# Kernel optimization log

Hardware: AMD Instinct MI355X
Metric: run time of the kernel (lower is better)

## Reference

```python
import jax, jax.numpy as jnp
import numpy as np

N_NODES = 50000
N_EDGES = 800000
D_IN = 256
D_OUT = 128
EPS = 1e-9


def setup_inputs() -> dict:
    key = jax.random.key(0)
    ks = jax.random.split(key, 6)
    feat = jax.random.normal(ks[0], (N_NODES, D_IN), dtype=jnp.float32)
    edge_row = jax.random.randint(ks[1], (N_EDGES,), 0, N_NODES)
    edge_col = jax.random.randint(ks[2], (N_EDGES,), 0, N_NODES)
    # normalized adjacency values (positive, ~1/degree scale)
    edge_val = jax.random.uniform(ks[3], (N_EDGES,), dtype=jnp.float32) / 16.0
    # xavier_uniform for Linear(dim_in, dim_out) weights, stored as [D_IN, D_OUT]
    limit = float(np.sqrt(6.0 / (D_IN + D_OUT)))
    W0 = jax.random.uniform(ks[4], (D_IN, D_OUT), minval=-limit, maxval=limit, dtype=jnp.float32)
    W1 = jax.random.uniform(ks[5], (D_IN, D_OUT), minval=-limit, maxval=limit, dtype=jnp.float32)
    zeros = jnp.zeros((D_OUT,), dtype=jnp.float32)
    ones = jnp.ones((D_OUT,), dtype=jnp.float32)
    return {
        "feat": feat,
        "W0": W0, "b0": zeros, "scale0": ones, "offset0": zeros,
        "W1": W1, "b1": zeros, "scale1": ones, "offset1": zeros,
        "edge_row": edge_row, "edge_col": edge_col, "edge_val": edge_val,
    }


def _spmm(edge_row, edge_col, edge_val, x):
    # out[r] += val * x[c] for each edge (r, c, val)  -- sparse adj @ x
    msgs = edge_val[:, None] * x[edge_col]  # [E, D]
    return jax.ops.segment_sum(msgs, edge_row, num_segments=N_NODES)


def _feat_trans(x, W, b, scale, offset):
    h = jax.nn.relu(x @ W + b)  # [N, D_OUT]
    mean = jnp.mean(h, axis=1, keepdims=True)
    var = jnp.var(h, axis=1, keepdims=True) + EPS  # unbiased=False (population var)
    return (h - mean) * scale * jax.lax.rsqrt(var) + offset


def reference(feat, W0, b0, scale0, offset0, W1, b1, scale1, offset1,
              edge_row, edge_col, edge_val):
    # non-first-layer path: feat_hop = [X, A @ X] (order=1), dropout p=0 is identity
    hop1 = _spmm(edge_row, edge_col, edge_val, feat)
    f0 = _feat_trans(feat, W0, b0, scale0, offset0)
    f1 = _feat_trans(hop1, W1, b1, scale1, offset1)
    return jnp.concatenate([f0, f1], axis=1)  # aggr == 'concat'
```

## Files before the change

kernel.cpp:

```cpp
#include <hip/hip_runtime.h>

#define N_NODES 50000
#define N_EDGES 800000
#define D_IN    256
#define D_OUT   128
#define EPS     1e-9f
#define CAP     64
#define PAD     88

#define SCATTER_BLOCKS 196
#define GEMM_MBLKS     391

typedef __attribute__((ext_vector_type(8))) short bf16x8;
typedef __attribute__((ext_vector_type(4))) float floatx4;

__device__ __forceinline__ ushort f2bf(float x) {
    unsigned u = __float_as_uint(x);
    u += 0x7fffu + ((u >> 16) & 1u);
    return (ushort)(u >> 16);
}

#define PREP_XB_BLOCKS  6250
#define PREP_WB_BLOCKS  32
__global__ __launch_bounds__(256) void prep(
    const float* __restrict__ feat, const float* __restrict__ W0,
    const float* __restrict__ W1, ushort* __restrict__ Xb,
    ushort* __restrict__ Wb)
{
    int bid = blockIdx.x;
    int t   = threadIdx.x;
    if (bid < PREP_XB_BLOCKS) {
        size_t g = (size_t)bid * 256 + t;
        const float* p = &feat[g * 8];
        float4 v0 = *(const float4*)p;
        float4 v1 = *(const float4*)(p + 4);
        union { ushort us[8]; uint4 v; } tmp;
        tmp.us[0] = f2bf(v0.x); tmp.us[1] = f2bf(v0.y);
        tmp.us[2] = f2bf(v0.z); tmp.us[3] = f2bf(v0.w);
        tmp.us[4] = f2bf(v1.x); tmp.us[5] = f2bf(v1.y);
        tmp.us[6] = f2bf(v1.z); tmp.us[7] = f2bf(v1.w);
        *(uint4*)&Xb[g * 8] = tmp.v;
    } else {
        int g  = (bid - PREP_XB_BLOCKS) * 256 + t;
        int n  = g >> 5;
        int kq = g & 31;
        const float* W = (n < 128) ? W0 : W1;
        int nn = n & 127;
        union { ushort us[8]; uint4 v; } tmp;
#pragma unroll
        for (int j = 0; j < 8; ++j)
            tmp.us[j] = f2bf(W[(size_t)(kq * 8 + j) * D_OUT + nn]);
        *(uint4*)&Wb[(size_t)n * D_IN + kq * 8] = tmp.v;
    }
}

__global__ __launch_bounds__(256, 3) void gemm_scatter(
    const ushort* __restrict__ Xb, const ushort* __restrict__ Wb,
    const float* __restrict__ bias, const float* __restrict__ scale,
    const float* __restrict__ offset,
    float* __restrict__ out, ushort* __restrict__ Y1,
    const int* __restrict__ er, const int* __restrict__ ec,
    const float* __restrict__ ev, int* __restrict__ cnt,
    int2* __restrict__ slot2)
{
    __shared__ ushort As[128 * PAD];
    __shared__ ushort Bs[128 * PAD];

    const int t = threadIdx.x;

    if (blockIdx.x < SCATTER_BLOCKS) {
        int ebase = blockIdx.x * 4096;
        int   rr[16], cc[16];
        float vv[16];
#pragma unroll
        for (int u = 0; u < 16; ++u) {
            int e = ebase + u * 256 + t;
            bool ok = (e < N_EDGES);
            rr[u] = ok ? er[e] : -1;
            cc[u] = ok ? ec[e] : 0;
            vv[u] = ok ? ev[e] : 0.f;
        }
#pragma unroll
        for (int u = 0; u < 16; ++u) {
            if (rr[u] >= 0) {
                int pos = atomicAdd(&cnt[rr[u]], 1);
                if (pos < CAP)
                    slot2[(size_t)rr[u] * CAP + pos] =
                        make_int2(cc[u], __float_as_int(vv[u]));
            }
        }
        return;
    }

    const int gbid = blockIdx.x - SCATTER_BLOCKS;
    const int half = gbid / GEMM_MBLKS;
    const int mblk = gbid % GEMM_MBLKS;
    const int wave = t >> 6, lane = t & 63;
    const int quad = lane >> 4, l16 = lane & 15;
    const int m0   = mblk * 128;
    const int n0   = half * 128;

    floatx4 acc[2][8];
#pragma unroll
    for (int mt = 0; mt < 2; ++mt)
#pragma unroll
        for (int nt = 0; nt < 8; ++nt)
            acc[mt][nt] = (floatx4){0.f, 0.f, 0.f, 0.f};

    for (int kt = 0; kt < D_IN; kt += 64) {
#pragma unroll
        for (int i = 0; i < 4; ++i) {
            int g = t + i * 256;
            int row = g >> 3, kq = g & 7;
            int grow = m0 + row;
            uint4 v = make_uint4(0u, 0u, 0u, 0u);
            if (grow < N_NODES)
                v = *(const uint4*)&Xb[(size_t)grow * D_IN + kt + kq * 8];
            *(uint4*)&As[row * PAD + kq * 8] = v;
        }
#pragma unroll
        for (int i = 0; i < 4; ++i) {
            int g = t + i * 256;
            int row = g >> 3, kq = g & 7;
            *(uint4*)&Bs[row * PAD + kq * 8] =
                *(const uint4*)&Wb[(size_t)(n0 + row) * D_IN + kt + kq * 8];
        }
        __syncthreads();

#pragma unroll
        for (int kk = 0; kk < 64; kk += 32) {
            bf16x8 a[2], b[8];
#pragma unroll
            for (int mt = 0; mt < 2; ++mt)
                a[mt] = *(bf16x8*)&As[(wave * 32 + mt * 16 + l16) * PAD + kk + quad * 8];
#pragma unroll
            for (int nt = 0; nt < 8; ++nt)
                b[nt] = *(bf16x8*)&Bs[(nt * 16 + l16) * PAD + kk + quad * 8];
#pragma unroll
            for (int mt = 0; mt < 2; ++mt)
#pragma unroll
                for (int nt = 0; nt < 8; ++nt)
                    acc[mt][nt] = __builtin_amdgcn_mfma_f32_16x16x32_bf16(
                        a[mt], b[nt], acc[mt][nt], 0, 0, 0);
        }
        __syncthreads();
    }

    if (half == 0) {
        float bb[8], sc[8], of[8];
#pragma unroll
        for (int nt = 0; nt < 8; ++nt) {
            bb[nt] = bias[nt * 16 + l16];
            sc[nt] = scale[nt * 16 + l16];
            of[nt] = offset[nt * 16 + l16];
        }
#pragma unroll
        for (int mt = 0; mt < 2; ++mt)
#pragma unroll
            for (int i = 0; i < 4; ++i) {
                float h[8], s = 0.f, q = 0.f;
#pragma unroll
                for (int nt = 0; nt < 8; ++nt) {
                    h[nt] = fmaxf(acc[mt][nt][i] + bb[nt], 0.f);
                    s += h[nt];
                    q += h[nt] * h[nt];
                }
#pragma unroll
                for (int m = 1; m < 16; m <<= 1) {
                    s += __shfl_xor(s, m);
                    q += __shfl_xor(q, m);
                }
                float mean = s * (1.f / 128.f);
                float inv  = rsqrtf(q * (1.f / 128.f) - mean * mean + EPS);
                int row = m0 + wave * 32 + mt * 16 + quad * 4 + i;
                if (row < N_NODES) {
#pragma unroll
                    for (int nt = 0; nt < 8; ++nt)
                        out[(size_t)row * 256 + nt * 16 + l16] =
                            (h[nt] - mean) * sc[nt] * inv + of[nt];
                }
            }
    } else {
#pragma unroll
        for (int mt = 0; mt < 2; ++mt)
#pragma unroll
            for (int i = 0; i < 4; ++i) {
                int row = m0 + wave * 32 + mt * 16 + quad * 4 + i;
                if (row < N_NODES) {
#pragma unroll
                    for (int nt = 0; nt < 8; ++nt)
                        Y1[(size_t)row * D_OUT + nt * 16 + l16] =
                            f2bf(acc[mt][nt][i]);
                }
            }
    }
}

__global__ __launch_bounds__(256) void spmm_gather_ln(
    const int* __restrict__ cnt, const int2* __restrict__ slot2,
    const ushort* __restrict__ Y,
    const float* __restrict__ bias, const float* __restrict__ scale,
    const float* __restrict__ offset, float* __restrict__ out)
{
    int row  = blockIdx.x * 4 + (threadIdx.x >> 6);
    int lane = threadIdx.x & 63;
    if (row >= N_NODES) return;

    int n = cnt[row];
    n = n < CAP ? n : CAP;

    int   c = 0;
    float v = 0.f;
    if (lane < n) {
        int2 p = slot2[(size_t)row * CAP + lane];
        c = p.x;
        v = __int_as_float(p.y);
    }

    float ax = 0.f, ay = 0.f;
    int j = 0;
    for (; j + 8 <= n; j += 8) {
        unsigned yv[8]; float vv[8];
#pragma unroll
        for (int u = 0; u < 8; ++u) {
            int cj = __shfl(c, j + u);
            vv[u]  = __shfl(v, j + u);
            yv[u]  = *(const unsigned*)&Y[(size_t)cj * D_OUT + lane * 2];
        }
#pragma unroll
        for (int u = 0; u < 8; ++u) {
            ax = fmaf(vv[u], __uint_as_float(yv[u] << 16), ax);
            ay = fmaf(vv[u], __uint_as_float(yv[u] & 0xffff0000u), ay);
        }
    }
    for (; j < n; ++j) {
        int   cj = __shfl(c, j);
        float vj = __shfl(v, j);
        unsigned yv = *(const unsigned*)&Y[(size_t)cj * D_OUT + lane * 2];
        ax = fmaf(vj, __uint_as_float(yv << 16), ax);
        ay = fmaf(vj, __uint_as_float(yv & 0xffff0000u), ay);
    }

    int cidx = lane * 2;
    float h0 = fmaxf(ax + bias[cidx + 0], 0.f);
    float h1 = fmaxf(ay + bias[cidx + 1], 0.f);
    float s = h0 + h1, q = h0 * h0 + h1 * h1;
#pragma unroll
    for (int m = 1; m < 64; m <<= 1) {
        s += __shfl_xor(s, m);
        q += __shfl_xor(q, m);
    }
    float mean = s * (1.f / 128.f);
    float var  = q * (1.f / 128.f) - mean * mean + EPS;
    float inv  = rsqrtf(var);
    float2 o;
    o.x = (h0 - mean) * scale[cidx + 0] * inv + offset[cidx + 0];
    o.y = (h1 - mean) * scale[cidx + 1] * inv + offset[cidx + 1];
    *(float2*)&out[(size_t)row * 256 + 128 + cidx] = o;
}

extern "C" void kernel_launch(void* const* d_in, const int* in_sizes, int n_in,
                              void* d_out, int out_size, void* d_ws, size_t ws_size,
                              hipStream_t stream)
{
    const float* feat = (const float*)d_in[0];
    const float* W0   = (const float*)d_in[1];
    const float* b0   = (const float*)d_in[2];
    const float* s0   = (const float*)d_in[3];
    const float* o0   = (const float*)d_in[4];
    const float* W1   = (const float*)d_in[5];
    const float* b1   = (const float*)d_in[6];
    const float* s1   = (const float*)d_in[7];
    const float* o1   = (const float*)d_in[8];
    const int*   er   = (const int*)d_in[9];
    const int*   ec   = (const int*)d_in[10];
    const float* ev   = (const float*)d_in[11];
    float* out = (float*)d_out;

    char*   wsb   = (char*)d_ws;
    ushort* Xb    = (ushort*)(wsb);
    ushort* Wb    = (ushort*)(wsb + 25600000);
    ushort* Y1    = (ushort*)(wsb + 25731072);
    int*    cnt   = (int*)   (wsb + 38531072);
    int2*   slot2 = (int2*)  (wsb + 38731072);

    hipMemsetAsync(cnt, 0, (size_t)N_NODES * sizeof(int), stream);

    prep<<<PREP_XB_BLOCKS + PREP_WB_BLOCKS, 256, 0, stream>>>(
        feat, W0, W1, Xb, Wb);

    gemm_scatter<<<SCATTER_BLOCKS + 2 * GEMM_MBLKS, 256, 0, stream>>>(
        Xb, Wb, b0, s0, o0, out, Y1, er, ec, ev, cnt, slot2);

    spmm_gather_ln<<<(N_NODES + 3) / 4, 256, 0, stream>>>(
        cnt, slot2, Y1, b1, s1, o1, out);
}
```

Baseline: 213.7 us.

## Fuse feature bf16 conversion into GEMM tile load and drop memset

```diff
diff --git a/kernel.cpp b/kernel.cpp
--- a/kernel.cpp
+++ b/kernel.cpp
@@ -20,28 +20,20 @@
     return (ushort)(u >> 16);
 }
 
-#define PREP_XB_BLOCKS  6250
-#define PREP_WB_BLOCKS  32
-__global__ __launch_bounds__(256) void prep(
-    const float* __restrict__ feat, const float* __restrict__ W0,
-    const float* __restrict__ W1, ushort* __restrict__ Xb,
-    ushort* __restrict__ Wb)
+#define CNT_BLOCKS 49
+#define WB_BLOCKS  32
+__global__ __launch_bounds__(256) void prep_small(
+    const float* __restrict__ W0, const float* __restrict__ W1,
+    ushort* __restrict__ Wb, int* __restrict__ cnt)
 {
     int bid = blockIdx.x;
     int t   = threadIdx.x;
-    if (bid < PREP_XB_BLOCKS) {
-        size_t g = (size_t)bid * 256 + t;
-        const float* p = &feat[g * 8];
-        float4 v0 = *(const float4*)p;
-        float4 v1 = *(const float4*)(p + 4);
-        union { ushort us[8]; uint4 v; } tmp;
-        tmp.us[0] = f2bf(v0.x); tmp.us[1] = f2bf(v0.y);
-        tmp.us[2] = f2bf(v0.z); tmp.us[3] = f2bf(v0.w);
-        tmp.us[4] = f2bf(v1.x); tmp.us[5] = f2bf(v1.y);
-        tmp.us[6] = f2bf(v1.z); tmp.us[7] = f2bf(v1.w);
-        *(uint4*)&Xb[g * 8] = tmp.v;
+    if (bid < CNT_BLOCKS) {
+        int idx4 = bid * 256 + t;
+        if (idx4 < 12500)
+            *(int4*)&cnt[idx4 * 4] = make_int4(0, 0, 0, 0);
     } else {
-        int g  = (bid - PREP_XB_BLOCKS) * 256 + t;
+        int g  = (bid - CNT_BLOCKS) * 256 + t;
         int n  = g >> 5;
         int kq = g & 31;
         const float* W = (n < 128) ? W0 : W1;
@@ -55,7 +47,7 @@
 }
 
 __global__ __launch_bounds__(256, 3) void gemm_scatter(
-    const ushort* __restrict__ Xb, const ushort* __restrict__ Wb,
+    const float* __restrict__ feat, const ushort* __restrict__ Wb,
     const float* __restrict__ bias, const float* __restrict__ scale,
     const float* __restrict__ offset,
     float* __restrict__ out, ushort* __restrict__ Y1,
@@ -113,10 +105,18 @@
             int g = t + i * 256;
             int row = g >> 3, kq = g & 7;
             int grow = m0 + row;
-            uint4 v = make_uint4(0u, 0u, 0u, 0u);
-            if (grow < N_NODES)
-                v = *(const uint4*)&Xb[(size_t)grow * D_IN + kt + kq * 8];
-            *(uint4*)&As[row * PAD + kq * 8] = v;
+            union { ushort us[8]; uint4 v; } tmp;
+            tmp.v = make_uint4(0u, 0u, 0u, 0u);
+            if (grow < N_NODES) {
+                const float* p = &feat[(size_t)grow * D_IN + kt + kq * 8];
+                float4 v0 = *(const float4*)p;
+                float4 v1 = *(const float4*)(p + 4);
+                tmp.us[0] = f2bf(v0.x); tmp.us[1] = f2bf(v0.y);
+                tmp.us[2] = f2bf(v0.z); tmp.us[3] = f2bf(v0.w);
+                tmp.us[4] = f2bf(v1.x); tmp.us[5] = f2bf(v1.y);
+                tmp.us[6] = f2bf(v1.z); tmp.us[7] = f2bf(v1.w);
+            }
+            *(uint4*)&As[row * PAD + kq * 8] = tmp.v;
         }
 #pragma unroll
         for (int i = 0; i < 4; ++i) {
@@ -278,19 +278,15 @@
     float* out = (float*)d_out;
 
     char*   wsb   = (char*)d_ws;
-    ushort* Xb    = (ushort*)(wsb);
-    ushort* Wb    = (ushort*)(wsb + 25600000);
-    ushort* Y1    = (ushort*)(wsb + 25731072);
-    int*    cnt   = (int*)   (wsb + 38531072);
-    int2*   slot2 = (int2*)  (wsb + 38731072);
-
-    hipMemsetAsync(cnt, 0, (size_t)N_NODES * sizeof(int), stream);
-
-    prep<<<PREP_XB_BLOCKS + PREP_WB_BLOCKS, 256, 0, stream>>>(
-        feat, W0, W1, Xb, Wb);
+    ushort* Wb    = (ushort*)(wsb);
+    ushort* Y1    = (ushort*)(wsb + 131072);
+    int*    cnt   = (int*)   (wsb + 12931072);
+    int2*   slot2 = (int2*)  (wsb + 13131072);
+
+    prep_small<<<CNT_BLOCKS + WB_BLOCKS, 256, 0, stream>>>(W0, W1, Wb, cnt);
 
     gemm_scatter<<<SCATTER_BLOCKS + 2 * GEMM_MBLKS, 256, 0, stream>>>(
-        Xb, Wb, b0, s0, o0, out, Y1, er, ec, ev, cnt, slot2);
+        feat, Wb, b0, s0, o0, out, Y1, er, ec, ev, cnt, slot2);
 
     spmm_gather_ln<<<(N_NODES + 3) / 4, 256, 0, stream>>>(
         cnt, slot2, Y1, b1, s1, o1, out);
```

New measurement: 209.5 us. 2.0% less time.
